# Kernel optimization log

Hardware: AMD Instinct MI355X
Metric: run time of the kernel (lower is better)

Reference implementation:

```python
import jax, jax.numpy as jnp
import numpy as np

B, T, I, H = 64, 512, 512, 1024  # batch, seq_len, input_size, hidden_size
G = 4 * H  # LSTM gate size


def setup_inputs() -> dict:
    key = jax.random.key(0)
    ks = jax.random.split(key, 9)
    s = 1.0 / np.sqrt(H)  # reset_parameters: uniform(-1/sqrt(H), 1/sqrt(H))
    u = lambda k, shape: jax.random.uniform(k, shape, jnp.float32, -s, s)
    return dict(
        x=jax.random.normal(ks[0], (B, T, I), jnp.float32),
        w_ih0=u(ks[1], (G, I)), w_hh0=u(ks[2], (G, H)),
        b_ih0=u(ks[3], (G,)), b_hh0=u(ks[4], (G,)),
        w_ih1=u(ks[5], (G, H)), w_hh1=u(ks[6], (G, H)),
        b_ih1=u(ks[7], (G,)), b_hh1=u(ks[8], (G,)),
        m_ih0=jnp.ones((G, I), bool), m_hh0=jnp.ones((G, H), bool),
        m_ih1=jnp.ones((G, H), bool), m_hh1=jnp.ones((G, H), bool),
    )


def _lstm_layer(x_tm, w_ih, w_hh, b_ih, b_hh, m_ih, m_hh):
    # x_tm: [T, B, in]; masked weights computed ONCE (the torch loop recomputes per step)
    wi = (w_ih * m_ih).T  # [in, 4H]
    wh = (w_hh * m_hh).T  # [H, 4H]
    Hh = w_hh.shape[1]
    h0 = jnp.zeros((x_tm.shape[1], Hh), x_tm.dtype)

    def step(carry, xt):
        h, c = carry
        gates = xt @ wi + b_ih + h @ wh + b_hh  # [B, 4H]
        i, f, g, o = jnp.split(gates, 4, axis=-1)  # chunk order: input, forget, cell, out
        c = jax.nn.sigmoid(f) * c + jax.nn.sigmoid(i) * jnp.tanh(g)
        h = jax.nn.sigmoid(o) * jnp.tanh(c)
        return (h, c), h

    _, ys = jax.lax.scan(step, (h0, h0), x_tm)
    return ys  # [T, B, H]


def reference(x, w_ih0, w_hh0, b_ih0, b_hh0, w_ih1, w_hh1, b_ih1, b_hh1,
              m_ih0, m_hh0, m_ih1, m_hh1):
    xt = jnp.swapaxes(x, 0, 1)  # time-major [T, B, I]
    y0 = _lstm_layer(xt, w_ih0, w_hh0, b_ih0, b_hh0, m_ih0, m_hh0)
    y1 = _lstm_layer(y0, w_ih1, w_hh1, b_ih1, b_hh1, m_ih1, m_hh1)
    return y1[-1]  # last timestep hidden of final layer: [B, H]
```

## Files before the change

kernel.cpp:

```cpp
#include <hip/hip_runtime.h>
#include <hip/hip_bf16.h>


#define B_ 64
#define T_ 512
#define I_ 512
#define H_ 1024
#define SH 65536
#define CSTR 16

typedef __attribute__((ext_vector_type(8))) short short8;
typedef __attribute__((ext_vector_type(4))) float f32x4;

static __device__ __forceinline__ ushort f2bf(float f) {
  __hip_bfloat16 h = __float2bfloat16(f);
  return *reinterpret_cast<ushort*>(&h);
}
static __device__ __forceinline__ float sigm(float v) {
  return 1.0f / (1.0f + expf(-v));
}
static __device__ __forceinline__ void store_short_wt(ushort* p, ushort v) {
  uint w = v;
  asm volatile("global_store_short %0, %1, off sc0 sc1" : : "v"(p), "v"(w) : "memory");
}
static __device__ __forceinline__ void store_int_wt(int* p, int v) {
  asm volatile("global_store_dword %0, %1, off sc0 sc1" : : "v"(p), "v"(v) : "memory");
}
template <typename T>
static __device__ __forceinline__ void pinv(T& x) {
  asm volatile("" : "+v"(x));
}
#define FW(base, t, s) ((base) + ((long)(t)*128 + (s)) * CSTR)
static __device__ __forceinline__ void pollgrp(int* base, long t, int g, int tgt,
                                               int lane) {
  int* w = FW(base, t, 4 * g + (lane & 3));
  if (__all(__hip_atomic_load(w, __ATOMIC_RELAXED, __HIP_MEMORY_SCOPE_AGENT) >= tgt))
    return;
  while (1) {
    __builtin_amdgcn_s_sleep(4);
    if (__all(__hip_atomic_load(w, __ATOMIC_RELAXED, __HIP_MEMORY_SCOPE_AGENT) >= tgt))
      return;
  }
}

__global__ void prep_x(const float* __restrict__ x, ushort* __restrict__ xtm, long n) {
  long idx = (long)blockIdx.x * blockDim.x + threadIdx.x;
  long stride = (long)gridDim.x * blockDim.x;
  for (; idx < n; idx += stride) {
    int i = (int)(idx % I_);
    long r = idx / I_;
    int b = (int)(r % B_);
    int t = (int)(r / B_);
    xtm[idx] = f2bf(x[(long)b * (T_ * I_) + (long)t * I_ + i]);
  }
}

__global__ void init_cnt(int* __restrict__ c, long n) {
  long i = (long)blockIdx.x * blockDim.x + threadIdx.x;
  long stride = (long)gridDim.x * blockDim.x;
  for (; i < n; i += stride) c[i] = 0;
}

#define MFMA16 __builtin_amdgcn_mfma_f32_16x16x32_bf16

template <int LAYER>
static __device__ __forceinline__ void run_layer(
    const ushort* __restrict__ xtm, ushort* __restrict__ y0, ushort* __restrict__ y1,
    int* __restrict__ flg0, int* __restrict__ flg1,
    const float* __restrict__ wih, const float* __restrict__ whh,
    const float* __restrict__ bih, const float* __restrict__ bhh,
    float* __restrict__ out, int sub, float* accx) {
  constexpr int K0 = LAYER ? H_ : I_;
  constexpr int NF = LAYER ? 8 : 6;

  const int hbase = sub * 8;
  const int tid = threadIdx.x;
  const int lane = tid & 63, wid = tid >> 6;
  const int l15 = lane & 15, khi = lane >> 4;

  short8 breg[2][NF];
#pragma unroll
  for (int cf = 0; cf < 2; ++cf)
#pragma unroll
    for (int jj = 0; jj < NF; ++jj) {
      int kcat;
      if (LAYER == 0)
        kcat = (jj < 2) ? (2 * wid + jj) * 32 : 512 + (4 * wid + jj - 2) * 32;
      else
        kcat = (jj < 4) ? (4 * wid + jj) * 32 : 1024 + (4 * wid + jj - 4) * 32;
      kcat += khi * 8;
      const int c = cf * 16 + l15;
      const int grow = (c >> 3) * H_ + hbase + (c & 7);
      const float* src = (kcat < K0) ? (wih + (long)grow * K0 + kcat)
                                     : (whh + (long)grow * H_ + (kcat - K0));
      float4 f0 = *(const float4*)src;
      float4 f1 = *(const float4*)(src + 4);
      short8 bv;
      bv[0] = (short)f2bf(f0.x); bv[1] = (short)f2bf(f0.y);
      bv[2] = (short)f2bf(f0.z); bv[3] = (short)f2bf(f0.w);
      bv[4] = (short)f2bf(f1.x); bv[5] = (short)f2bf(f1.y);
      bv[6] = (short)f2bf(f1.z); bv[7] = (short)f2bf(f1.w);
      breg[cf][jj] = bv;
    }
#pragma unroll
  for (int cf = 0; cf < 2; ++cf)
#pragma unroll
    for (int jj = 0; jj < NF; ++jj) pinv(breg[cf][jj]);

  const int brow = tid >> 3, hc = tid & 7;
  float bs[4];
#pragma unroll
  for (int g = 0; g < 4; ++g)
    bs[g] = bih[g * H_ + hbase + hc] + bhh[g * H_ + hbase + hc];
  float creg = 0.0f;

  ushort* ymine = LAYER ? y1 : y0;
  int* flgMy = LAYER ? flg1 : flg0;

  for (int t = 0; t < T_; ++t) {
    f32x4 acc[4][2] = {};

    if (LAYER == 0) {
      {
        short8 a[2][4];
        const ushort* px = xtm + (long)t * (B_ * I_) + khi * 8;
#pragma unroll
        for (int jj = 0; jj < 2; ++jj)
#pragma unroll
          for (int mt = 0; mt < 4; ++mt)
            a[jj][mt] = *(const short8*)(px + (long)(mt * 16 + l15) * I_ +
                                         (2 * wid + jj) * 32);
#pragma unroll
        for (int jj = 0; jj < 2; ++jj)
#pragma unroll
          for (int mt = 0; mt < 4; ++mt) pinv(a[jj][mt]);
        __builtin_amdgcn_sched_barrier(0);
#pragma unroll
        for (int jj = 0; jj < 2; ++jj)
#pragma unroll
          for (int mt = 0; mt < 4; ++mt) {
            acc[mt][0] = MFMA16(a[jj][mt], breg[0][jj], acc[mt][0], 0, 0, 0);
            acc[mt][1] = MFMA16(a[jj][mt], breg[1][jj], acc[mt][1], 0, 0, 0);
          }
      }
      if (t > 0) {
        short8 a[4][4];
        const ushort* ph = y0 + (long)(t - 1) * SH;
#pragma unroll
        for (int jj = 0; jj < 4; ++jj) {
          pollgrp(flg0, t - 1, 4 * wid + jj, t, lane);
#pragma unroll
          for (int mt = 0; mt < 4; ++mt) {
            const int slice = (4 * wid + jj) * 4 + khi;
            a[jj][mt] = *(const short8*)(ph + ((long)slice * 64 + mt * 16 + l15) * 8);
          }
        }
#pragma unroll
        for (int jj = 0; jj < 4; ++jj)
#pragma unroll
          for (int mt = 0; mt < 4; ++mt) pinv(a[jj][mt]);
        __builtin_amdgcn_sched_barrier(0);
#pragma unroll
        for (int jj = 0; jj < 4; ++jj)
#pragma unroll
          for (int mt = 0; mt < 4; ++mt) {
            acc[mt][0] = MFMA16(a[jj][mt], breg[0][jj + 2], acc[mt][0], 0, 0, 0);
            acc[mt][1] = MFMA16(a[jj][mt], breg[1][jj + 2], acc[mt][1], 0, 0, 0);
          }
      }
    } else {
      {
        short8 a[4][4];
        const ushort* pa = y0 + (long)t * SH;
#pragma unroll
        for (int jj = 0; jj < 4; ++jj) {
          pollgrp(flg0, t, 4 * wid + jj, t + 1, lane);
#pragma unroll
          for (int mt = 0; mt < 4; ++mt) {
            const int slice = (4 * wid + jj) * 4 + khi;
            a[jj][mt] = *(const short8*)(pa + ((long)slice * 64 + mt * 16 + l15) * 8);
          }
        }
#pragma unroll
        for (int jj = 0; jj < 4; ++jj)
#pragma unroll
          for (int mt = 0; mt < 4; ++mt) pinv(a[jj][mt]);
        __builtin_amdgcn_sched_barrier(0);
#pragma unroll
        for (int jj = 0; jj < 4; ++jj)
#pragma unroll
          for (int mt = 0; mt < 4; ++mt) {
            acc[mt][0] = MFMA16(a[jj][mt], breg[0][jj], acc[mt][0], 0, 0, 0);
            acc[mt][1] = MFMA16(a[jj][mt], breg[1][jj], acc[mt][1], 0, 0, 0);
          }
      }
      if (t > 0) {
        short8 a[4][4];
        const ushort* ph = y1 + (long)(t - 1) * SH;
#pragma unroll
        for (int jj = 0; jj < 4; ++jj) {
          pollgrp(flg1, t - 1, 4 * wid + jj, t, lane);
#pragma unroll
          for (int mt = 0; mt < 4; ++mt) {
            const int slice = (4 * wid + jj) * 4 + khi;
            a[jj][mt] = *(const short8*)(ph + ((long)slice * 64 + mt * 16 + l15) * 8);
          }
        }
#pragma unroll
        for (int jj = 0; jj < 4; ++jj)
#pragma unroll
          for (int mt = 0; mt < 4; ++mt) pinv(a[jj][mt]);
        __builtin_amdgcn_sched_barrier(0);
#pragma unroll
        for (int jj = 0; jj < 4; ++jj)
#pragma unroll
          for (int mt = 0; mt < 4; ++mt) {
            acc[mt][0] = MFMA16(a[jj][mt], breg[0][jj + 4], acc[mt][0], 0, 0, 0);
            acc[mt][1] = MFMA16(a[jj][mt], breg[1][jj + 4], acc[mt][1], 0, 0, 0);
          }
      }
    }

#pragma unroll
    for (int mt = 0; mt < 4; ++mt)
#pragma unroll
      for (int cf = 0; cf < 2; ++cf)
        *(f32x4*)&accx[(((wid * 4 + mt) * 32) + (cf * 16 + l15)) * 20 + khi * 4] =
            acc[mt][cf];
    __syncthreads();

    {
      const int mt2 = brow >> 4, rr = brow & 15;
      float gv[4];
#pragma unroll
      for (int g = 0; g < 4; ++g) {
        const int c = g * 8 + hc;
        float s = bs[g];
#pragma unroll
        for (int w = 0; w < 8; ++w)
          s += accx[((w * 4 + mt2) * 32 + c) * 20 + rr];
        gv[g] = s;
      }
      float cn = sigm(gv[1]) * creg + sigm(gv[0]) * tanhf(gv[2]);
      float hn = sigm(gv[3]) * tanhf(cn);
      creg = cn;
      store_short_wt(ymine + (long)t * SH + sub * 512 + tid, f2bf(hn));
      if (LAYER == 1 && t == T_ - 1) out[(long)brow * H_ + hbase + hc] = hn;
    }
    asm volatile("s_waitcnt vmcnt(0)" ::: "memory");
    __syncthreads();
    if (tid == 0) store_int_wt(FW(flgMy, t, sub), t + 1);
  }
}

__global__ __launch_bounds__(512, 1) void lstm_persist(
    const ushort* __restrict__ xtm, ushort* __restrict__ y0, ushort* __restrict__ y1,
    int* __restrict__ flg,
    const float* __restrict__ wih0, const float* __restrict__ whh0,
    const float* __restrict__ bih0, const float* __restrict__ bhh0,
    const float* __restrict__ wih1, const float* __restrict__ whh1,
    const float* __restrict__ bih1, const float* __restrict__ bhh1,
    float* __restrict__ out) {
  __shared__ float accx[8 * 4 * 32 * 20];
  const int wg = blockIdx.x;
  int* flg0 = flg;
  int* flg1 = flg + (long)T_ * 128 * CSTR;
  if (wg < 128)
    run_layer<0>(xtm, y0, y1, flg0, flg1, wih0, whh0, bih0, bhh0, out, wg, accx);
  else
    run_layer<1>(xtm, y0, y1, flg0, flg1, wih1, whh1, bih1, bhh1, out, wg - 128,
                 accx);
}

extern "C" void kernel_launch(void* const* d_in, const int* in_sizes, int n_in,
                              void* d_out, int out_size, void* d_ws, size_t ws_size,
                              hipStream_t stream) {
  const float* x    = (const float*)d_in[0];
  const float* wih0 = (const float*)d_in[1];
  const float* whh0 = (const float*)d_in[2];
  const float* bih0 = (const float*)d_in[3];
  const float* bhh0 = (const float*)d_in[4];
  const float* wih1 = (const float*)d_in[5];
  const float* whh1 = (const float*)d_in[6];
  const float* bih1 = (const float*)d_in[7];
  const float* bhh1 = (const float*)d_in[8];

  const long szX = (long)B_ * T_ * I_ * 2;
  const long szY = (long)T_ * SH * 2;
  const long szF = (long)2 * T_ * 128 * CSTR * 4;

  char* p = (char*)d_ws;
  ushort* xtm = (ushort*)p;  p += szX;
  ushort* y0  = (ushort*)p;  p += szY;
  ushort* y1  = (ushort*)p;  p += szY;
  int*    flg = (int*)p;     p += szF;
  float* outp = (float*)d_out;

  prep_x<<<2048, 256, 0, stream>>>(x, xtm, (long)B_ * T_ * I_);
  init_cnt<<<2048, 256, 0, stream>>>(flg, szF / 4);

  void* args[] = {
    (void*)&xtm, (void*)&y0, (void*)&y1, (void*)&flg,
    (void*)&wih0, (void*)&whh0, (void*)&bih0, (void*)&bhh0,
    (void*)&wih1, (void*)&whh1, (void*)&bih1, (void*)&bhh1,
    (void*)&outp,
  };
  hipLaunchCooperativeKernel((const void*)lstm_persist, dim3(256), dim3(512),
                             args, 0, stream);
}
```

Before: 2.566 ms.

## Split batch into two independent halves with 16-wide hidden slices per block

```diff
diff --git a/kernel.cpp b/kernel.cpp
--- a/kernel.cpp
+++ b/kernel.cpp
@@ -6,7 +6,7 @@
 #define T_ 512
 #define I_ 512
 #define H_ 1024
-#define SH 65536
+#define SHH 32768
 #define CSTR 16
 
 typedef __attribute__((ext_vector_type(8))) short short8;
@@ -30,10 +30,10 @@
 static __device__ __forceinline__ void pinv(T& x) {
   asm volatile("" : "+v"(x));
 }
-#define FW(base, t, s) ((base) + ((long)(t)*128 + (s)) * CSTR)
-static __device__ __forceinline__ void pollgrp(int* base, long t, int g, int tgt,
-                                               int lane) {
-  int* w = FW(base, t, 4 * g + (lane & 3));
+#define FW(base, t, s) ((base) + ((long)(t)*64 + (s)) * CSTR)
+static __device__ __forceinline__ void pollgrp2(int* base, long t, int p0, int tgt,
+                                                int lane) {
+  int* w = FW(base, t, p0 + (lane & 1));
   if (__all(__hip_atomic_load(w, __ATOMIC_RELAXED, __HIP_MEMORY_SCOPE_AGENT) >= tgt))
     return;
   while (1) {
@@ -63,34 +63,53 @@
 
 #define MFMA16 __builtin_amdgcn_mfma_f32_16x16x32_bf16
 
+#define CONSUME_PART(YH, TT, TAGV, FLG, JB)                                    \
+  {                                                                            \
+    short8 a[4][2];                                                            \
+    _Pragma("unroll") for (int jj = 0; jj < 4; ++jj) {                         \
+      pollgrp2(FLG, TT, wid * 8 + jj * 2, TAGV, lane);                         \
+      const int slice = wid * 8 + jj * 2 + (khi >> 1);                         \
+      _Pragma("unroll") for (int mt = 0; mt < 2; ++mt)                         \
+          a[jj][mt] = *(const short8*)((YH) + (long)(TT)*SHH + slice * 512 +   \
+                                       (mt * 16 + l15) * 16 + (khi & 1) * 8);  \
+    }                                                                          \
+    _Pragma("unroll") for (int jj = 0; jj < 4; ++jj)                           \
+        _Pragma("unroll") for (int mt = 0; mt < 2; ++mt) pinv(a[jj][mt]);      \
+    __builtin_amdgcn_sched_barrier(0);                                         \
+    _Pragma("unroll") for (int jj = 0; jj < 4; ++jj)                           \
+        _Pragma("unroll") for (int mt = 0; mt < 2; ++mt)                       \
+            _Pragma("unroll") for (int cf = 0; cf < 4; ++cf)                   \
+                acc[mt][cf] =                                                  \
+                    MFMA16(a[jj][mt], breg[cf][jj + JB], acc[mt][cf], 0, 0, 0);\
+  }
+
 template <int LAYER>
 static __device__ __forceinline__ void run_layer(
-    const ushort* __restrict__ xtm, ushort* __restrict__ y0, ushort* __restrict__ y1,
-    int* __restrict__ flg0, int* __restrict__ flg1,
+    const ushort* __restrict__ xtm, ushort* __restrict__ y0h,
+    ushort* __restrict__ y1h, int* __restrict__ flg0h, int* __restrict__ flg1h,
     const float* __restrict__ wih, const float* __restrict__ whh,
     const float* __restrict__ bih, const float* __restrict__ bhh,
-    float* __restrict__ out, int sub, float* accx) {
+    float* __restrict__ out, int half, int sub, float* accx) {
   constexpr int K0 = LAYER ? H_ : I_;
   constexpr int NF = LAYER ? 8 : 6;
 
-  const int hbase = sub * 8;
+  const int hbase = sub * 16;
   const int tid = threadIdx.x;
   const int lane = tid & 63, wid = tid >> 6;
   const int l15 = lane & 15, khi = lane >> 4;
 
-  short8 breg[2][NF];
-#pragma unroll
-  for (int cf = 0; cf < 2; ++cf)
+  short8 breg[4][NF];
+#pragma unroll
+  for (int cf = 0; cf < 4; ++cf)
 #pragma unroll
     for (int jj = 0; jj < NF; ++jj) {
       int kcat;
       if (LAYER == 0)
-        kcat = (jj < 2) ? (2 * wid + jj) * 32 : 512 + (4 * wid + jj - 2) * 32;
+        kcat = (jj < 2) ? (2 * wid + jj) * 32 : 512 + (wid * 128 + (jj - 2) * 32);
       else
-        kcat = (jj < 4) ? (4 * wid + jj) * 32 : 1024 + (4 * wid + jj - 4) * 32;
+        kcat = (jj < 4) ? (wid * 128 + jj * 32) : 1024 + (wid * 128 + (jj - 4) * 32);
       kcat += khi * 8;
-      const int c = cf * 16 + l15;
-      const int grow = (c >> 3) * H_ + hbase + (c & 7);
+      const int grow = cf * H_ + hbase + l15;
       const float* src = (kcat < K0) ? (wih + (long)grow * K0 + kcat)
                                      : (whh + (long)grow * H_ + (kcat - K0));
       float4 f0 = *(const float4*)src;
@@ -103,149 +122,78 @@
       breg[cf][jj] = bv;
     }
 #pragma unroll
-  for (int cf = 0; cf < 2; ++cf)
+  for (int cf = 0; cf < 4; ++cf)
 #pragma unroll
     for (int jj = 0; jj < NF; ++jj) pinv(breg[cf][jj]);
 
-  const int brow = tid >> 3, hc = tid & 7;
+  const int row = tid >> 4, c16 = tid & 15;
   float bs[4];
 #pragma unroll
   for (int g = 0; g < 4; ++g)
-    bs[g] = bih[g * H_ + hbase + hc] + bhh[g * H_ + hbase + hc];
+    bs[g] = bih[g * H_ + hbase + c16] + bhh[g * H_ + hbase + c16];
   float creg = 0.0f;
 
-  ushort* ymine = LAYER ? y1 : y0;
-  int* flgMy = LAYER ? flg1 : flg0;
+  ushort* ymine = LAYER ? y1h : y0h;
+  int* flgMy = LAYER ? flg1h : flg0h;
 
   for (int t = 0; t < T_; ++t) {
-    f32x4 acc[4][2] = {};
+    f32x4 acc[2][4] = {};
 
     if (LAYER == 0) {
       {
-        short8 a[2][4];
-        const ushort* px = xtm + (long)t * (B_ * I_) + khi * 8;
+        short8 a[2][2];
+        const ushort* px =
+            xtm + (long)t * (B_ * I_) + (long)(half * 32) * I_ + khi * 8;
 #pragma unroll
         for (int jj = 0; jj < 2; ++jj)
 #pragma unroll
-          for (int mt = 0; mt < 4; ++mt)
+          for (int mt = 0; mt < 2; ++mt)
             a[jj][mt] = *(const short8*)(px + (long)(mt * 16 + l15) * I_ +
                                          (2 * wid + jj) * 32);
 #pragma unroll
         for (int jj = 0; jj < 2; ++jj)
 #pragma unroll
-          for (int mt = 0; mt < 4; ++mt) pinv(a[jj][mt]);
+          for (int mt = 0; mt < 2; ++mt) pinv(a[jj][mt]);
         __builtin_amdgcn_sched_barrier(0);
 #pragma unroll
         for (int jj = 0; jj < 2; ++jj)
 #pragma unroll
-          for (int mt = 0; mt < 4; ++mt) {
-            acc[mt][0] = MFMA16(a[jj][mt], breg[0][jj], acc[mt][0], 0, 0, 0);
-            acc[mt][1] = MFMA16(a[jj][mt], breg[1][jj], acc[mt][1], 0, 0, 0);
-          }
+          for (int mt = 0; mt < 2; ++mt)
+#pragma unroll
+            for (int cf = 0; cf < 4; ++cf)
+              acc[mt][cf] = MFMA16(a[jj][mt], breg[cf][jj], acc[mt][cf], 0, 0, 0);
       }
-      if (t > 0) {
-        short8 a[4][4];
-        const ushort* ph = y0 + (long)(t - 1) * SH;
-#pragma unroll
-        for (int jj = 0; jj < 4; ++jj) {
-          pollgrp(flg0, t - 1, 4 * wid + jj, t, lane);
-#pragma unroll
-          for (int mt = 0; mt < 4; ++mt) {
-            const int slice = (4 * wid + jj) * 4 + khi;
-            a[jj][mt] = *(const short8*)(ph + ((long)slice * 64 + mt * 16 + l15) * 8);
-          }
-        }
-#pragma unroll
-        for (int jj = 0; jj < 4; ++jj)
-#pragma unroll
-          for (int mt = 0; mt < 4; ++mt) pinv(a[jj][mt]);
-        __builtin_amdgcn_sched_barrier(0);
-#pragma unroll
-        for (int jj = 0; jj < 4; ++jj)
-#pragma unroll
-          for (int mt = 0; mt < 4; ++mt) {
-            acc[mt][0] = MFMA16(a[jj][mt], breg[0][jj + 2], acc[mt][0], 0, 0, 0);
-            acc[mt][1] = MFMA16(a[jj][mt], breg[1][jj + 2], acc[mt][1], 0, 0, 0);
-          }
-      }
+      if (t > 0) CONSUME_PART(y0h, t - 1, t, flg0h, 2);
     } else {
-      {
-        short8 a[4][4];
-        const ushort* pa = y0 + (long)t * SH;
-#pragma unroll
-        for (int jj = 0; jj < 4; ++jj) {
-          pollgrp(flg0, t, 4 * wid + jj, t + 1, lane);
-#pragma unroll
-          for (int mt = 0; mt < 4; ++mt) {
-            const int slice = (4 * wid + jj) * 4 + khi;
-            a[jj][mt] = *(const short8*)(pa + ((long)slice * 64 + mt * 16 + l15) * 8);
-          }
-        }
-#pragma unroll
-        for (int jj = 0; jj < 4; ++jj)
-#pragma unroll
-          for (int mt = 0; mt < 4; ++mt) pinv(a[jj][mt]);
-        __builtin_amdgcn_sched_barrier(0);
-#pragma unroll
-        for (int jj = 0; jj < 4; ++jj)
-#pragma unroll
-          for (int mt = 0; mt < 4; ++mt) {
-            acc[mt][0] = MFMA16(a[jj][mt], breg[0][jj], acc[mt][0], 0, 0, 0);
-            acc[mt][1] = MFMA16(a[jj][mt], breg[1][jj], acc[mt][1], 0, 0, 0);
-          }
-      }
-      if (t > 0) {
-        short8 a[4][4];
-        const ushort* ph = y1 + (long)(t - 1) * SH;
-#pragma unroll
-        for (int jj = 0; jj < 4; ++jj) {
-          pollgrp(flg1, t - 1, 4 * wid + jj, t, lane);
-#pragma unroll
-          for (int mt = 0; mt < 4; ++mt) {
-            const int slice = (4 * wid + jj) * 4 + khi;
-            a[jj][mt] = *(const short8*)(ph + ((long)slice * 64 + mt * 16 + l15) * 8);
-          }
-        }
-#pragma unroll
-        for (int jj = 0; jj < 4; ++jj)
-#pragma unroll
-          for (int mt = 0; mt < 4; ++mt) pinv(a[jj][mt]);
-        __builtin_amdgcn_sched_barrier(0);
-#pragma unroll
-        for (int jj = 0; jj < 4; ++jj)
-#pragma unroll
-          for (int mt = 0; mt < 4; ++mt) {
-            acc[mt][0] = MFMA16(a[jj][mt], breg[0][jj + 4], acc[mt][0], 0, 0, 0);
-            acc[mt][1] = MFMA16(a[jj][mt], breg[1][jj + 4], acc[mt][1], 0, 0, 0);
-          }
-      }
+      CONSUME_PART(y0h, t, t + 1, flg0h, 0);
+      if (t > 0) CONSUME_PART(y1h, t - 1, t, flg1h, 4);
     }
 
 #pragma unroll
-    for (int mt = 0; mt < 4; ++mt)
-#pragma unroll
-      for (int cf = 0; cf < 2; ++cf)
-        *(f32x4*)&accx[(((wid * 4 + mt) * 32) + (cf * 16 + l15)) * 20 + khi * 4] =
+    for (int mt = 0; mt < 2; ++mt)
+#pragma unroll
+      for (int cf = 0; cf < 4; ++cf)
+        *(f32x4*)&accx[(((wid * 2 + mt) * 64) + (cf * 16 + l15)) * 20 + khi * 4] =
             acc[mt][cf];
     __syncthreads();
 
     {
-      const int mt2 = brow >> 4, rr = brow & 15;
+      const int mt2 = row >> 4, rr = row & 15;
       float gv[4];
 #pragma unroll
       for (int g = 0; g < 4; ++g) {
-        const int c = g * 8 + hc;
         float s = bs[g];
 #pragma unroll
         for (int w = 0; w < 8; ++w)
-          s += accx[((w * 4 + mt2) * 32 + c) * 20 + rr];
+          s += accx[((w * 2 + mt2) * 64 + g * 16 + c16) * 20 + rr];
         gv[g] = s;
       }
       float cn = sigm(gv[1]) * creg + sigm(gv[0]) * tanhf(gv[2]);
       float hn = sigm(gv[3]) * tanhf(cn);
       creg = cn;
-      store_short_wt(ymine + (long)t * SH + sub * 512 + tid, f2bf(hn));
-      if (LAYER == 1 && t == T_ - 1) out[(long)brow * H_ + hbase + hc] = hn;
+      store_short_wt(ymine + (long)t * SHH + sub * 512 + tid, f2bf(hn));
+      if (LAYER == 1 && t == T_ - 1)
+        out[(long)(half * 32 + row) * H_ + hbase + c16] = hn;
     }
     asm volatile("s_waitcnt vmcnt(0)" ::: "memory");
     __syncthreads();
@@ -261,15 +209,22 @@
     const float* __restrict__ wih1, const float* __restrict__ whh1,
     const float* __restrict__ bih1, const float* __restrict__ bhh1,
     float* __restrict__ out) {
-  __shared__ float accx[8 * 4 * 32 * 20];
+  __shared__ float accx[16 * 64 * 20];
   const int wg = blockIdx.x;
-  int* flg0 = flg;
-  int* flg1 = flg + (long)T_ * 128 * CSTR;
-  if (wg < 128)
-    run_layer<0>(xtm, y0, y1, flg0, flg1, wih0, whh0, bih0, bhh0, out, wg, accx);
+  const int layer = wg >> 7;
+  const int half = (wg >> 6) & 1;
+  const int sub = wg & 63;
+  const long fsz = (long)T_ * 64 * CSTR;
+  ushort* y0h = y0 + (long)half * T_ * SHH;
+  ushort* y1h = y1 + (long)half * T_ * SHH;
+  int* flg0h = flg + (long)half * fsz;
+  int* flg1h = flg + (long)(2 + half) * fsz;
+  if (layer == 0)
+    run_layer<0>(xtm, y0h, y1h, flg0h, flg1h, wih0, whh0, bih0, bhh0, out, half,
+                 sub, accx);
   else
-    run_layer<1>(xtm, y0, y1, flg0, flg1, wih1, whh1, bih1, bhh1, out, wg - 128,
-                 accx);
+    run_layer<1>(xtm, y0h, y1h, flg0h, flg1h, wih1, whh1, bih1, bhh1, out, half,
+                 sub, accx);
 }
 
 extern "C" void kernel_launch(void* const* d_in, const int* in_sizes, int n_in,
@@ -286,8 +241,8 @@
   const float* bhh1 = (const float*)d_in[8];
 
   const long szX = (long)B_ * T_ * I_ * 2;
-  const long szY = (long)T_ * SH * 2;
-  const long szF = (long)2 * T_ * 128 * CSTR * 4;
+  const long szY = (long)2 * T_ * SHH * 2;
+  const long szF = (long)4 * T_ * 64 * CSTR * 4;
 
   char* p = (char*)d_ws;
   ushort* xtm = (ushort*)p;  p += szX;
```

After: 2.485 ms. 3.2% less time.
